# Optimization experiments

Hardware: AMD Instinct MI355X
Metric: run time of the kernel (lower is better)

The kernel has to match this reference:

```python
import jax, jax.numpy as jnp
import numpy as np

HEADS = 8
KD = 64  # key_dim
VD = 64  # value_dim


def _conv1x1(W, b, x):
    # 1x1 conv == per-pixel matmul over channels. W: [out, in], x: [b, in, h, w]
    return jnp.einsum('oc,bchw->bohw', W, x) + b[:, None, None]


def setup_inputs() -> dict:
    key = jax.random.key(0)
    ks = jax.random.split(key, 9)
    B, C, H, W = 4, 128, 128, 128
    s = 0.02
    return {
        'x':  jax.random.normal(ks[0], (B, C, H, W), jnp.float32),
        'Wq': jax.random.normal(ks[1], (KD * HEADS, C), jnp.float32) * s,
        'bq': jax.random.normal(ks[2], (KD * HEADS,), jnp.float32) * s,
        'Wk': jax.random.normal(ks[3], (KD * HEADS, C), jnp.float32) * s,
        'bk': jax.random.normal(ks[4], (KD * HEADS,), jnp.float32) * s,
        'Wv': jax.random.normal(ks[5], (VD * HEADS, C), jnp.float32) * s,
        'bv': jax.random.normal(ks[6], (VD * HEADS,), jnp.float32) * s,
        'Wo': jax.random.normal(ks[7], (C, VD * HEADS), jnp.float32) * s,
        'bo': jax.random.normal(ks[8], (C,), jnp.float32) * s,
    }


def reference(x, Wq, bq, Wk, bk, Wv, bv, Wo, bo):
    B, C, H, W = x.shape
    n = H * W
    scale = KD ** -0.25
    # projections -> [b, heads, dim, n]
    q = _conv1x1(Wq, bq, x).reshape(B, HEADS, KD, n) * scale
    k = _conv1x1(Wk, bk, x).reshape(B, HEADS, KD, n) * scale
    v = _conv1x1(Wv, bv, x).reshape(B, HEADS, VD, n)
    # linear attention: softmax k over tokens (n), softmax q over key dim (d)
    k = jax.nn.softmax(k, axis=-1)
    q = jax.nn.softmax(q, axis=-2)
    ctx = jnp.einsum('bhdn,bhen->bhde', k, v)   # [b, h, kd, vd] small context
    out = jnp.einsum('bhdn,bhde->bhen', q, ctx)  # [b, h, vd, n]
    out = out.reshape(B, HEADS * VD, H, W)
    return _conv1x1(Wo, bo, out)
```

## Files before the change

kernel.cpp:

```cpp
#include <hip/hip_runtime.h>

typedef unsigned short u16;
typedef __bf16 bf16x8 __attribute__((ext_vector_type(8)));
typedef float f32x4 __attribute__((ext_vector_type(4)));

#define N_ 16384
#define SCALE 0.35355339059327379f

__device__ __forceinline__ u16 f2bf(float f){
  union { float f; unsigned int i; } v; v.f = f;
  unsigned int b = v.i;
  return (u16)((b + 0x7FFFu + ((b >> 16) & 1u)) >> 16);
}
__device__ __forceinline__ unsigned int pack2bf(float a, float b){
  return ((unsigned int)f2bf(b) << 16) | (unsigned int)f2bf(a);
}

__global__ __launch_bounds__(256) void prep(const float* __restrict__ Wq,
    const float* __restrict__ bq, const float* __restrict__ Wk,
    const float* __restrict__ bk, const float* __restrict__ Wv,
    const float* __restrict__ bv, u16* __restrict__ wkvf, u16* __restrict__ wqf,
    float* __restrict__ bkv, float* __restrict__ bqs){
  const int T = blockIdx.x * 256 + threadIdx.x;
  if (T < 1024){
    int jj = T & 127, h = T >> 7;
    bkv[T] = (jj < 64) ? SCALE * bk[h * 64 + jj] : bv[h * 64 + jj - 64];
  } else if (T < 1536){
    bqs[T - 1024] = SCALE * bq[T - 1024];
  }
  const float* src; float sc; u16* dst;
  if (T < 16384){
    int l = T & 63, f = T >> 6;
    int ks = f & 3, jt = (f >> 2) & 7, h = f >> 5;
    int jj = 16 * jt + (l & 15);
    int k0 = ks * 32 + (l >> 4) * 8;
    if (jj < 64){ src = Wk + (size_t)(h * 64 + jj) * 128 + k0; sc = SCALE; }
    else        { src = Wv + (size_t)(h * 64 + jj - 64) * 128 + k0; sc = 1.f; }
    dst = wkvf + (size_t)f * 512 + l * 8;
  } else {
    int T2 = T - 16384;
    int l = T2 & 63, f = T2 >> 6;
    int ks = f & 3, dt = (f >> 2) & 3, h = f >> 4;
    int d = 16 * dt + (l & 15);
    int k0 = ks * 32 + (l >> 4) * 8;
    src = Wq + (size_t)(h * 64 + d) * 128 + k0; sc = SCALE;
    dst = wqf + (size_t)f * 512 + l * 8;
  }
  float4 a = *(const float4*)src, c = *(const float4*)(src + 4);
  ushort4 o0, o1;
  o0.x = f2bf(sc * a.x); o0.y = f2bf(sc * a.y); o0.z = f2bf(sc * a.z); o0.w = f2bf(sc * a.w);
  o1.x = f2bf(sc * c.x); o1.y = f2bf(sc * c.y); o1.z = f2bf(sc * c.z); o1.w = f2bf(sc * c.w);
  *(ushort4*)dst = o0; *(ushort4*)(dst + 4) = o1;
}

__global__ __launch_bounds__(256) void convx(const float* __restrict__ x,
                                             u16* __restrict__ xt){
  const int tid = threadIdx.x;
  const int b = blockIdx.y;
  const int kq = tid >> 6;
  const int t0 = blockIdx.x * 128 + 2 * (tid & 63);
  const float* xp = x + (size_t)(b * 128 + kq * 32) * N_ + t0;
  u16* dst = xt + (size_t)(b * N_ + t0) * 128;
#pragma unroll
  for (int gi = 0; gi < 4; gi++){
    float2 v[8];
#pragma unroll
    for (int j = 0; j < 8; j++)
      v[j] = *(const float2*)(xp + (size_t)(gi * 8 + j) * N_);
    const int g = kq * 4 + gi;
    {
      uint4 o;
      o.x = pack2bf(v[0].x, v[1].x); o.y = pack2bf(v[2].x, v[3].x);
      o.z = pack2bf(v[4].x, v[5].x); o.w = pack2bf(v[6].x, v[7].x);
      *(uint4*)(dst + ((g ^ (t0 & 15)) * 8)) = o;
    }
    {
      uint4 o;
      o.x = pack2bf(v[0].y, v[1].y); o.y = pack2bf(v[2].y, v[3].y);
      o.z = pack2bf(v[4].y, v[5].y); o.w = pack2bf(v[6].y, v[7].y);
      const int t = t0 + 1;
      *(uint4*)(dst + 128 + ((g ^ (t & 15)) * 8)) = o;
    }
  }
}

__global__ __launch_bounds__(256, 2) void kvctx(const u16* __restrict__ xt,
    const u16* __restrict__ wkvf, const float* __restrict__ bkv,
    float* __restrict__ pctx, float* __restrict__ prs){
  __shared__ u16 smem[32768];
  const int tid = threadIdx.x;
  const int chunk = blockIdx.x, h = blockIdx.y, b = blockIdx.z;
  const int w = tid >> 6, l = tid & 63, r15 = l & 15, q = l >> 4;
  const int th = w & 1, jh = w >> 1;

  bf16x8 wf[4][4];
#pragma unroll
  for (int ni = 0; ni < 4; ni++)
#pragma unroll
    for (int ks = 0; ks < 4; ks++)
      wf[ni][ks] = *(const bf16x8*)(wkvf +
          (size_t)((h * 8 + 4 * jh + ni) * 4 + ks) * 512 + l * 8);
  float barr[4];
#pragma unroll
  for (int ni = 0; ni < 4; ni++)
    barr[ni] = bkv[h * 128 + jh * 64 + 16 * ni + r15];

  const size_t tok0 = (size_t)b * N_ + chunk * 512;
  const char* gbase = (const char*)(xt + tok0 * 128);
  u16* sekv = smem + 16384;

#define STAGE(sub_)                                                            \
  {                                                                            \
    const char* gs = gbase + (size_t)(sub_)*32768 + w * 8192 + l * 16;         \
    char* ls = (char*)smem + w * 8192;                                         \
    _Pragma("unroll")                                                          \
    for (int p = 0; p < 8; p++)                                                \
      __builtin_amdgcn_global_load_lds(                                        \
          (const __attribute__((address_space(1))) void*)(gs + p * 1024),      \
          (__attribute__((address_space(3))) void*)(ls + p * 1024), 16, 0, 0); \
  }

  STAGE(0);
  __syncthreads();

  f32x4 acc2[4][4] = {};
  float rs[4] = {0.f, 0.f, 0.f, 0.f};

  for (int sub = 0; sub < 4; sub++){
    f32x4 acc1[4][4] = {};
#pragma unroll
    for (int ks = 0; ks < 4; ks++){
      bf16x8 xa[4];
#pragma unroll
      for (int mi = 0; mi < 4; mi++){
        int t = th * 64 + 16 * mi + r15;
        xa[mi] = *(const bf16x8*)&smem[t * 128 + (((ks * 4 + q) ^ r15) * 8)];
      }
#pragma unroll
      for (int mi = 0; mi < 4; mi++)
#pragma unroll
        for (int ni = 0; ni < 4; ni++)
          acc1[mi][ni] = __builtin_amdgcn_mfma_f32_16x16x32_bf16(
              xa[mi], wf[ni][ks], acc1[mi][ni], 0, 0, 0);
    }
#pragma unroll
    for (int ni = 0; ni < 4; ni++){
      const float bb = barr[ni];
      const int j = jh * 64 + 16 * ni + r15;
      float ps = 0.f;
#pragma unroll
      for (int mi = 0; mi < 4; mi++){
        float vals[4];
#pragma unroll
        for (int r = 0; r < 4; r++) vals[r] = acc1[mi][ni][r] + bb;
        if (jh == 0){
#pragma unroll
          for (int r = 0; r < 4; r++){ vals[r] = __expf(vals[r]); ps += vals[r]; }
        }
        uint2 pk;
        pk.x = pack2bf(vals[0], vals[1]);
        pk.y = pack2bf(vals[2], vals[3]);
        int g8 = 16 * th + 4 * mi + q;
        int g8s = g8 ^ (2 * r15);
        *(uint2*)&sekv[j * 128 + g8s * 4] = pk;
      }
      if (jh == 0){
        ps += __shfl_xor(ps, 16); ps += __shfl_xor(ps, 32);
        rs[ni] += ps;
      }
    }
    __syncthreads();
    if (sub < 3) STAGE(sub + 1);
    {
      bf16x8 ka[4], va[4];
      const int g8s = (8 * w + 2 * q) ^ (2 * r15);
#pragma unroll
      for (int mi2 = 0; mi2 < 4; mi2++){
        int d = 16 * mi2 + r15;
        ka[mi2] = *(const bf16x8*)&sekv[d * 128 + g8s * 4];
      }
#pragma unroll
      for (int ni2 = 0; ni2 < 4; ni2++){
        int e = 16 * ni2 + r15;
        va[ni2] = *(const bf16x8*)&sekv[(64 + e) * 128 + g8s * 4];
      }
#pragma unroll
      for (int mi2 = 0; mi2 < 4; mi2++)
#pragma unroll
        for (int ni2 = 0; ni2 < 4; ni2++)
          acc2[mi2][ni2] = __builtin_amdgcn_mfma_f32_16x16x32_bf16(
              ka[mi2], va[ni2], acc2[mi2][ni2], 0, 0, 0);
    }
    __syncthreads();
  }
#undef STAGE
  float* fb = (float*)smem;
#pragma unroll
  for (int mi2 = 0; mi2 < 4; mi2++)
#pragma unroll
    for (int ni2 = 0; ni2 < 4; ni2++)
#pragma unroll
      for (int r = 0; r < 4; r++){
        int d = 16 * mi2 + 4 * q + r, e = 16 * ni2 + r15;
        fb[w * 4096 + d * 64 + e] = acc2[mi2][ni2][r];
      }
  __syncthreads();
  {
    float* dst = pctx + ((size_t)((b * 8 + h) * 32 + chunk)) * 4096 + tid * 16;
#pragma unroll
    for (int i = 0; i < 4; i++){
      int o = tid * 16 + 4 * i;
      float4 a = *(const float4*)(fb + o);
      float4 c = *(const float4*)(fb + 4096 + o);
      float4 d = *(const float4*)(fb + 8192 + o);
      float4 e = *(const float4*)(fb + 12288 + o);
      float4 s;
      s.x = a.x + c.x + d.x + e.x; s.y = a.y + c.y + d.y + e.y;
      s.z = a.z + c.z + d.z + e.z; s.w = a.w + c.w + d.w + e.w;
      *(float4*)(dst + 4 * i) = s;
    }
  }
  if (jh == 0 && q == 0){
    float* rb = prs + ((size_t)((b * 8 + h) * 32 + chunk)) * 128 + th * 64;
#pragma unroll
    for (int ni = 0; ni < 4; ni++) rb[16 * ni + r15] = rs[ni];
  }
}

__global__ __launch_bounds__(256) void ctxred(const float* __restrict__ pctx,
    const float* __restrict__ prs, float* __restrict__ ctx,
    float* __restrict__ rowsum){
  const int bh = blockIdx.x, s = blockIdx.y, tid = threadIdx.x;
  const float2* base = (const float2*)(pctx + (size_t)bh * 32 * 4096 + s * 512) + tid;
  float2 acc = {0.f, 0.f};
#pragma unroll 4
  for (int t = 0; t < 32; t++){
    float2 v = base[t * 2048];
    acc.x += v.x; acc.y += v.y;
  }
  *((float2*)(ctx + (size_t)bh * 4096 + s * 512) + tid) = acc;
  if (s == 0 && tid < 64){
    const float* rb = prs + (size_t)bh * 32 * 128 + tid;
    float sm = 0.f;
    for (int t = 0; t < 32; t++) sm += rb[t * 128] + rb[t * 128 + 64];
    rowsum[bh * 64 + tid] = sm;
  }
}

__global__ __launch_bounds__(256) void mker(const float* __restrict__ ctx,
    const float* __restrict__ Wo, const float* __restrict__ rowsum,
    u16* __restrict__ mtf){
  __shared__ float ctxh[64][68];
  __shared__ float woht[64][132];
  const int tid = threadIdx.x;
  const int h = blockIdx.x, b = blockIdx.y;
  const int bh = b * 8 + h;
  const int e4 = tid & 15, r0 = tid >> 4;
#pragma unroll
  for (int p = 0; p < 4; p++){
    int d = r0 + p * 16;
    float4 v = *(const float4*)(ctx + ((size_t)bh * 64 + d) * 64 + 4 * e4);
    *(float4*)&ctxh[d][4 * e4] = v;
  }
#pragma unroll
  for (int p = 0; p < 8; p++){
    int c = r0 + p * 16;
    float4 v = *(const float4*)(Wo + (size_t)c * 512 + h * 64 + 4 * e4);
    woht[4 * e4 + 0][c] = v.x; woht[4 * e4 + 1][c] = v.y;
    woht[4 * e4 + 2][c] = v.z; woht[4 * e4 + 3][c] = v.w;
  }
  __syncthreads();
  const int cg = tid & 3, d = tid >> 2;
  const float inv = 1.f / rowsum[bh * 64 + d];
  float acc[32];
#pragma unroll
  for (int cc = 0; cc < 32; cc++) acc[cc] = 0.f;
  for (int e = 0; e < 64; e++){
    float cv = ctxh[d][e];
#pragma unroll
    for (int cc = 0; cc < 32; cc++) acc[cc] += cv * woht[e][cg + 4 * cc];
  }
  const int ks = d >> 5, lq = ((d >> 3) & 3) << 4, el = d & 7;
#pragma unroll
  for (int cc = 0; cc < 32; cc++){
    int c = cg + 4 * cc;
    mtf[((size_t)(bh * 8 + (c >> 4)) * 2 + ks) * 512 + ((c & 15) | lq) * 8 + el]
        = f2bf(inv * acc[cc]);
  }
}

__global__ __launch_bounds__(256, 3) void qout(const u16* __restrict__ xt,
    const u16* __restrict__ wqf, const float* __restrict__ bqs,
    const u16* __restrict__ mtf, const float* __restrict__ bo,
    float* __restrict__ out){
  __shared__ u16 smP[4][16 * 64];
  const int tid = threadIdx.x;
  const int tt = blockIdx.x, b = blockIdx.y;
  const int w = tid >> 6, l = tid & 63, r15 = l & 15, q = l >> 4;
  const int t0 = tt * 64;
  const int m7 = 2 * (r15 & 7);
  const int t = t0 + w * 16 + r15;

  bf16x8 xb[4];
#pragma unroll
  for (int ks = 0; ks < 4; ks++)
    xb[ks] = *(const bf16x8*)(xt + (size_t)(b * N_ + t) * 128 +
                              (((ks * 4 + q) ^ r15) * 8));

  u16* sp = smP[w];
  f32x4 acc3[8] = {};
  for (int h = 0; h < 8; h++){
    float bq_[4][4];
#pragma unroll
    for (int mi = 0; mi < 4; mi++){
      float4 v = *(const float4*)(bqs + h * 64 + 16 * mi + 4 * q);
      bq_[mi][0] = v.x; bq_[mi][1] = v.y; bq_[mi][2] = v.z; bq_[mi][3] = v.w;
    }
    f32x4 acc1[4] = {};
#pragma unroll
    for (int ks = 0; ks < 4; ks++){
      bf16x8 wqv[4];
#pragma unroll
      for (int mi = 0; mi < 4; mi++)
        wqv[mi] = *(const bf16x8*)(wqf +
            (size_t)((h * 4 + mi) * 4 + ks) * 512 + l * 8);
#pragma unroll
      for (int mi = 0; mi < 4; mi++)
        acc1[mi] = __builtin_amdgcn_mfma_f32_16x16x32_bf16(
            wqv[mi], xb[ks], acc1[mi], 0, 0, 0);
    }
    {
      float ps = 0.f;
#pragma unroll
      for (int mi = 0; mi < 4; mi++)
#pragma unroll
        for (int r = 0; r < 4; r++){
          float e = __expf(acc1[mi][r] + bq_[mi][r]);
          acc1[mi][r] = e; ps += e;
        }
      ps += __shfl_xor(ps, 16); ps += __shfl_xor(ps, 32);
      const float ci = 1.f / ps;
#pragma unroll
      for (int mi = 0; mi < 4; mi++){
        uint2 pk;
        pk.x = pack2bf(acc1[mi][0] * ci, acc1[mi][1] * ci);
        pk.y = pack2bf(acc1[mi][2] * ci, acc1[mi][3] * ci);
        int g8s = (4 * mi + q) ^ m7;
        *(uint2*)&sp[r15 * 64 + g8s * 4] = pk;
      }
    }
#pragma unroll
    for (int ks2 = 0; ks2 < 2; ks2++){
      const int g8s = (8 * ks2 + 2 * q) ^ m7;
      bf16x8 pb = *(const bf16x8*)&sp[r15 * 64 + g8s * 4];
#pragma unroll
      for (int half = 0; half < 2; half++){
        bf16x8 mf[4];
#pragma unroll
        for (int mm = 0; mm < 4; mm++)
          mf[mm] = *(const bf16x8*)(mtf +
              ((size_t)((b * 8 + h) * 8 + half * 4 + mm) * 2 + ks2) * 512 + l * 8);
#pragma unroll
        for (int mm = 0; mm < 4; mm++)
          acc3[half * 4 + mm] = __builtin_amdgcn_mfma_f32_16x16x32_bf16(
              mf[mm], pb, acc3[half * 4 + mm], 0, 0, 0);
      }
    }
  }
#pragma unroll
  for (int mi = 0; mi < 8; mi++){
    float4 bv = *(const float4*)(bo + 16 * mi + 4 * q);
    float bs[4] = {bv.x, bv.y, bv.z, bv.w};
#pragma unroll
    for (int r = 0; r < 4; r++){
      int c = 16 * mi + 4 * q + r;
      out[(size_t)(b * 128 + c) * N_ + t] = acc3[mi][r] + bs[r];
    }
  }
}

extern "C" void kernel_launch(void* const* d_in, const int* in_sizes, int n_in,
                              void* d_out, int out_size, void* d_ws, size_t ws_size,
                              hipStream_t stream){
  const float* x  = (const float*)d_in[0];
  const float* Wq = (const float*)d_in[1];
  const float* bq = (const float*)d_in[2];
  const float* Wk = (const float*)d_in[3];
  const float* bk = (const float*)d_in[4];
  const float* Wv = (const float*)d_in[5];
  const float* bv = (const float*)d_in[6];
  const float* Wo = (const float*)d_in[7];
  const float* bo = (const float*)d_in[8];
  float* out = (float*)d_out;

  char* ws = (char*)d_ws;
  u16*   xt     = (u16*)ws;
  u16*   wkvf   = (u16*)(ws + 16777216);
  u16*   wqf    = (u16*)(ws + 17039360);
  u16*   mtf    = (u16*)(ws + 17170432);
  float* bkv    = (float*)(ws + 17694720);
  float* bqs    = (float*)(ws + 17698816);
  float* rowsum = (float*)(ws + 17700864);
  float* ctx    = (float*)(ws + 17709056);
  float* pctx   = (float*)(ws + 18233344);
  float* prs    = (float*)(ws + 35010560);

  prep <<<96, 256, 0, stream>>>(Wq, bq, Wk, bk, Wv, bv, wkvf, wqf, bkv, bqs);
  convx<<<dim3(128, 4), 256, 0, stream>>>(x, xt);
  kvctx<<<dim3(32, 8, 4), 256, 0, stream>>>(xt, wkvf, bkv, pctx, prs);
  ctxred<<<dim3(32, 8), 256, 0, stream>>>(pctx, prs, ctx, rowsum);
  mker <<<dim3(8, 4), 256, 0, stream>>>(ctx, Wo, rowsum, mtf);
  qout <<<dim3(256, 4), 256, 0, stream>>>(xt, wqf, bqs, mtf, bo, out);
}
```

Baseline: 202.8 us.

## Merge prep/convx and ctxred/mker kernels, software-pipeline qout heads, use hw bf16 cvt

Folds the weight-prep and x-transpose kernels into one launch, and folds the partial-context reduction into the M-matrix kernel, removing two launches and the ctx/rowsum round trips through global memory. Replaces the manual bf16 rounding with the v_cvt_pk_bf16_f32 instruction. In kvctx, the next-stage load is moved earlier between split barriers. qout is double-buffered across head pairs so the Q projection of the next head overlaps the softmax and output MFMA of the current one, and its occupancy hint is raised to 4. The redmker reduction now runs on only 32 blocks, which may serialize the pctx reads, and the extra live accumulators in qout add register pressure.

```diff
diff --git a/kernel.cpp b/kernel.cpp
--- a/kernel.cpp
+++ b/kernel.cpp
@@ -12,16 +12,50 @@
   unsigned int b = v.i;
   return (u16)((b + 0x7FFFu + ((b >> 16) & 1u)) >> 16);
 }
-__device__ __forceinline__ unsigned int pack2bf(float a, float b){
-  return ((unsigned int)f2bf(b) << 16) | (unsigned int)f2bf(a);
-}
-
-__global__ __launch_bounds__(256) void prep(const float* __restrict__ Wq,
+__device__ __forceinline__ unsigned int cvtpk(float a, float b){
+  unsigned int r;
+  asm("v_cvt_pk_bf16_f32 %0, %1, %2" : "=v"(r) : "v"(a), "v"(b));
+  return r;
+}
+
+__global__ __launch_bounds__(256) void pconvx(const float* __restrict__ x,
+    u16* __restrict__ xt, const float* __restrict__ Wq,
     const float* __restrict__ bq, const float* __restrict__ Wk,
     const float* __restrict__ bk, const float* __restrict__ Wv,
     const float* __restrict__ bv, u16* __restrict__ wkvf, u16* __restrict__ wqf,
     float* __restrict__ bkv, float* __restrict__ bqs){
-  const int T = blockIdx.x * 256 + threadIdx.x;
+  const int tid = threadIdx.x;
+  const int bid = blockIdx.x;
+  if (bid < 512){
+    const int b = bid >> 7;
+    const int kq = tid >> 6;
+    const int t0 = (bid & 127) * 128 + 2 * (tid & 63);
+    const float* xp = x + (size_t)(b * 128 + kq * 32) * N_ + t0;
+    u16* dst = xt + (size_t)(b * N_ + t0) * 128;
+#pragma unroll
+    for (int gi = 0; gi < 4; gi++){
+      float2 v[8];
+#pragma unroll
+      for (int j = 0; j < 8; j++)
+        v[j] = *(const float2*)(xp + (size_t)(gi * 8 + j) * N_);
+      const int g = kq * 4 + gi;
+      {
+        uint4 o;
+        o.x = cvtpk(v[0].x, v[1].x); o.y = cvtpk(v[2].x, v[3].x);
+        o.z = cvtpk(v[4].x, v[5].x); o.w = cvtpk(v[6].x, v[7].x);
+        *(uint4*)(dst + ((g ^ (t0 & 15)) * 8)) = o;
+      }
+      {
+        uint4 o;
+        o.x = cvtpk(v[0].y, v[1].y); o.y = cvtpk(v[2].y, v[3].y);
+        o.z = cvtpk(v[4].y, v[5].y); o.w = cvtpk(v[6].y, v[7].y);
+        const int t = t0 + 1;
+        *(uint4*)(dst + 128 + ((g ^ (t & 15)) * 8)) = o;
+      }
+    }
+    return;
+  }
+  const int T = (bid - 512) * 256 + tid;
   if (T < 1024){
     int jj = T & 127, h = T >> 7;
     bkv[T] = (jj < 64) ? SCALE * bk[h * 64 + jj] : bv[h * 64 + jj - 64];
@@ -53,37 +87,6 @@
   *(ushort4*)dst = o0; *(ushort4*)(dst + 4) = o1;
 }
 
-__global__ __launch_bounds__(256) void convx(const float* __restrict__ x,
-                                             u16* __restrict__ xt){
-  const int tid = threadIdx.x;
-  const int b = blockIdx.y;
-  const int kq = tid >> 6;
-  const int t0 = blockIdx.x * 128 + 2 * (tid & 63);
-  const float* xp = x + (size_t)(b * 128 + kq * 32) * N_ + t0;
-  u16* dst = xt + (size_t)(b * N_ + t0) * 128;
-#pragma unroll
-  for (int gi = 0; gi < 4; gi++){
-    float2 v[8];
-#pragma unroll
-    for (int j = 0; j < 8; j++)
-      v[j] = *(const float2*)(xp + (size_t)(gi * 8 + j) * N_);
-    const int g = kq * 4 + gi;
-    {
-      uint4 o;
-      o.x = pack2bf(v[0].x, v[1].x); o.y = pack2bf(v[2].x, v[3].x);
-      o.z = pack2bf(v[4].x, v[5].x); o.w = pack2bf(v[6].x, v[7].x);
-      *(uint4*)(dst + ((g ^ (t0 & 15)) * 8)) = o;
-    }
-    {
-      uint4 o;
-      o.x = pack2bf(v[0].y, v[1].y); o.y = pack2bf(v[2].y, v[3].y);
-      o.z = pack2bf(v[4].y, v[5].y); o.w = pack2bf(v[6].y, v[7].y);
-      const int t = t0 + 1;
-      *(uint4*)(dst + 128 + ((g ^ (t & 15)) * 8)) = o;
-    }
-  }
-}
-
 __global__ __launch_bounds__(256, 2) void kvctx(const u16* __restrict__ xt,
     const u16* __restrict__ wkvf, const float* __restrict__ bkv,
     float* __restrict__ pctx, float* __restrict__ prs){
@@ -143,6 +146,9 @@
           acc1[mi][ni] = __builtin_amdgcn_mfma_f32_16x16x32_bf16(
               xa[mi], wf[ni][ks], acc1[mi][ni], 0, 0, 0);
     }
+    asm volatile("s_waitcnt lgkmcnt(0)" ::: "memory");
+    __builtin_amdgcn_s_barrier();
+    if (sub < 3) STAGE(sub + 1);
 #pragma unroll
     for (int ni = 0; ni < 4; ni++){
       const float bb = barr[ni];
@@ -158,8 +164,8 @@
           for (int r = 0; r < 4; r++){ vals[r] = __expf(vals[r]); ps += vals[r]; }
         }
         uint2 pk;
-        pk.x = pack2bf(vals[0], vals[1]);
-        pk.y = pack2bf(vals[2], vals[3]);
+        pk.x = cvtpk(vals[0], vals[1]);
+        pk.y = cvtpk(vals[2], vals[3]);
         int g8 = 16 * th + 4 * mi + q;
         int g8s = g8 ^ (2 * r15);
         *(uint2*)&sekv[j * 128 + g8s * 4] = pk;
@@ -169,8 +175,8 @@
         rs[ni] += ps;
       }
     }
-    __syncthreads();
-    if (sub < 3) STAGE(sub + 1);
+    asm volatile("s_waitcnt lgkmcnt(0)" ::: "memory");
+    __builtin_amdgcn_s_barrier();
     {
       bf16x8 ka[4], va[4];
       const int g8s = (8 * w + 2 * q) ^ (2 * r15);
@@ -227,51 +233,53 @@
   }
 }
 
-__global__ __launch_bounds__(256) void ctxred(const float* __restrict__ pctx,
-    const float* __restrict__ prs, float* __restrict__ ctx,
-    float* __restrict__ rowsum){
-  const int bh = blockIdx.x, s = blockIdx.y, tid = threadIdx.x;
-  const float2* base = (const float2*)(pctx + (size_t)bh * 32 * 4096 + s * 512) + tid;
-  float2 acc = {0.f, 0.f};
-#pragma unroll 4
-  for (int t = 0; t < 32; t++){
-    float2 v = base[t * 2048];
-    acc.x += v.x; acc.y += v.y;
-  }
-  *((float2*)(ctx + (size_t)bh * 4096 + s * 512) + tid) = acc;
-  if (s == 0 && tid < 64){
-    const float* rb = prs + (size_t)bh * 32 * 128 + tid;
-    float sm = 0.f;
-    for (int t = 0; t < 32; t++) sm += rb[t * 128] + rb[t * 128 + 64];
-    rowsum[bh * 64 + tid] = sm;
-  }
-}
-
-__global__ __launch_bounds__(256) void mker(const float* __restrict__ ctx,
-    const float* __restrict__ Wo, const float* __restrict__ rowsum,
+__global__ __launch_bounds__(256) void redmker(const float* __restrict__ pctx,
+    const float* __restrict__ prs, const float* __restrict__ Wo,
     u16* __restrict__ mtf){
   __shared__ float ctxh[64][68];
   __shared__ float woht[64][132];
+  __shared__ float rsh[64];
   const int tid = threadIdx.x;
-  const int h = blockIdx.x, b = blockIdx.y;
-  const int bh = b * 8 + h;
-  const int e4 = tid & 15, r0 = tid >> 4;
-#pragma unroll
-  for (int p = 0; p < 4; p++){
-    int d = r0 + p * 16;
-    float4 v = *(const float4*)(ctx + ((size_t)bh * 64 + d) * 64 + 4 * e4);
-    *(float4*)&ctxh[d][4 * e4] = v;
-  }
-#pragma unroll
-  for (int p = 0; p < 8; p++){
-    int c = r0 + p * 16;
-    float4 v = *(const float4*)(Wo + (size_t)c * 512 + h * 64 + 4 * e4);
-    woht[4 * e4 + 0][c] = v.x; woht[4 * e4 + 1][c] = v.y;
-    woht[4 * e4 + 2][c] = v.z; woht[4 * e4 + 3][c] = v.w;
+  const int bh = blockIdx.x;
+  const int h = bh & 7;
+  {
+    const int e4 = tid & 15, r0 = tid >> 4;
+#pragma unroll
+    for (int p = 0; p < 8; p++){
+      int c = r0 + p * 16;
+      float4 v = *(const float4*)(Wo + (size_t)c * 512 + h * 64 + 4 * e4);
+      woht[4 * e4 + 0][c] = v.x; woht[4 * e4 + 1][c] = v.y;
+      woht[4 * e4 + 2][c] = v.z; woht[4 * e4 + 3][c] = v.w;
+    }
+  }
+  {
+    const float4* base = (const float4*)(pctx + (size_t)bh * 131072) + tid * 4;
+    float4 a0 = {0,0,0,0}, a1 = {0,0,0,0}, a2 = {0,0,0,0}, a3 = {0,0,0,0};
+#pragma unroll 4
+    for (int c = 0; c < 32; c++){
+      float4 v0 = base[c * 1024 + 0], v1 = base[c * 1024 + 1];
+      float4 v2 = base[c * 1024 + 2], v3 = base[c * 1024 + 3];
+      a0.x += v0.x; a0.y += v0.y; a0.z += v0.z; a0.w += v0.w;
+      a1.x += v1.x; a1.y += v1.y; a1.z += v1.z; a1.w += v1.w;
+      a2.x += v2.x; a2.y += v2.y; a2.z += v2.z; a2.w += v2.w;
+      a3.x += v3.x; a3.y += v3.y; a3.z += v3.z; a3.w += v3.w;
+    }
+    const int d = tid >> 2, e0 = (tid & 3) * 16;
+    *(float4*)&ctxh[d][e0 + 0]  = a0;
+    *(float4*)&ctxh[d][e0 + 4]  = a1;
+    *(float4*)&ctxh[d][e0 + 8]  = a2;
+    *(float4*)&ctxh[d][e0 + 12] = a3;
+  }
+  if (tid < 64){
+    const float* rb = prs + (size_t)bh * 4096 + tid;
+    float sm = 0.f;
+#pragma unroll 4
+    for (int c = 0; c < 32; c++) sm += rb[c * 128] + rb[c * 128 + 64];
+    rsh[tid] = sm;
   }
   __syncthreads();
   const int cg = tid & 3, d = tid >> 2;
-  const float inv = 1.f / rowsum[bh * 64 + d];
+  const float inv = 1.f / rsh[d];
   float acc[32];
 #pragma unroll
   for (int cc = 0; cc < 32; cc++) acc[cc] = 0.f;
@@ -289,11 +297,11 @@
   }
 }
 
-__global__ __launch_bounds__(256, 3) void qout(const u16* __restrict__ xt,
+__global__ __launch_bounds__(256, 4) void qout(const u16* __restrict__ xt,
     const u16* __restrict__ wqf, const float* __restrict__ bqs,
     const u16* __restrict__ mtf, const float* __restrict__ bo,
     float* __restrict__ out){
-  __shared__ u16 smP[4][16 * 64];
+  __shared__ u16 smP[4][2][16 * 64];
   const int tid = threadIdx.x;
   const int tt = blockIdx.x, b = blockIdx.y;
   const int w = tid >> 6, l = tid & 63, r15 = l & 15, q = l >> 4;
@@ -307,66 +315,83 @@
     xb[ks] = *(const bf16x8*)(xt + (size_t)(b * N_ + t) * 128 +
                               (((ks * 4 + q) ^ r15) * 8));
 
-  u16* sp = smP[w];
+  u16* sp0 = smP[w][0];
+  u16* sp1 = smP[w][1];
   f32x4 acc3[8] = {};
-  for (int h = 0; h < 8; h++){
-    float bq_[4][4];
-#pragma unroll
-    for (int mi = 0; mi < 4; mi++){
-      float4 v = *(const float4*)(bqs + h * 64 + 16 * mi + 4 * q);
-      bq_[mi][0] = v.x; bq_[mi][1] = v.y; bq_[mi][2] = v.z; bq_[mi][3] = v.w;
-    }
-    f32x4 acc1[4] = {};
-#pragma unroll
-    for (int ks = 0; ks < 4; ks++){
-      bf16x8 wqv[4];
-#pragma unroll
-      for (int mi = 0; mi < 4; mi++)
-        wqv[mi] = *(const bf16x8*)(wqf +
-            (size_t)((h * 4 + mi) * 4 + ks) * 512 + l * 8);
-#pragma unroll
-      for (int mi = 0; mi < 4; mi++)
-        acc1[mi] = __builtin_amdgcn_mfma_f32_16x16x32_bf16(
-            wqv[mi], xb[ks], acc1[mi], 0, 0, 0);
-    }
-    {
-      float ps = 0.f;
-#pragma unroll
-      for (int mi = 0; mi < 4; mi++)
-#pragma unroll
-        for (int r = 0; r < 4; r++){
-          float e = __expf(acc1[mi][r] + bq_[mi][r]);
-          acc1[mi][r] = e; ps += e;
-        }
-      ps += __shfl_xor(ps, 16); ps += __shfl_xor(ps, 32);
-      const float ci = 1.f / ps;
-#pragma unroll
-      for (int mi = 0; mi < 4; mi++){
-        uint2 pk;
-        pk.x = pack2bf(acc1[mi][0] * ci, acc1[mi][1] * ci);
-        pk.y = pack2bf(acc1[mi][2] * ci, acc1[mi][3] * ci);
-        int g8s = (4 * mi + q) ^ m7;
-        *(uint2*)&sp[r15 * 64 + g8s * 4] = pk;
-      }
-    }
-#pragma unroll
-    for (int ks2 = 0; ks2 < 2; ks2++){
-      const int g8s = (8 * ks2 + 2 * q) ^ m7;
-      bf16x8 pb = *(const bf16x8*)&sp[r15 * 64 + g8s * 4];
-#pragma unroll
-      for (int half = 0; half < 2; half++){
-        bf16x8 mf[4];
-#pragma unroll
-        for (int mm = 0; mm < 4; mm++)
-          mf[mm] = *(const bf16x8*)(mtf +
-              ((size_t)((b * 8 + h) * 8 + half * 4 + mm) * 2 + ks2) * 512 + l * 8);
-#pragma unroll
-        for (int mm = 0; mm < 4; mm++)
-          acc3[half * 4 + mm] = __builtin_amdgcn_mfma_f32_16x16x32_bf16(
-              mf[mm], pb, acc3[half * 4 + mm], 0, 0, 0);
-      }
-    }
-  }
+
+#define MFMA1(h_, acc_)                                                      \
+  { _Pragma("unroll")                                                        \
+    for (int ks = 0; ks < 4; ks++){                                          \
+      bf16x8 wqv[4];                                                         \
+      _Pragma("unroll")                                                      \
+      for (int mi = 0; mi < 4; mi++)                                         \
+        wqv[mi] = *(const bf16x8*)(wqf +                                     \
+            (size_t)(((h_) * 4 + mi) * 4 + ks) * 512 + l * 8);               \
+      _Pragma("unroll")                                                      \
+      for (int mi = 0; mi < 4; mi++)                                         \
+        acc_[mi] = __builtin_amdgcn_mfma_f32_16x16x32_bf16(                  \
+            wqv[mi], xb[ks], acc_[mi], 0, 0, 0);                             \
+    } }
+
+#define SM(h_, acc_, sp_)                                                    \
+  { float ps = 0.f;                                                          \
+    _Pragma("unroll")                                                        \
+    for (int mi = 0; mi < 4; mi++){                                          \
+      float4 bv = *(const float4*)(bqs + (h_) * 64 + 16 * mi + 4 * q);       \
+      float e0 = __expf(acc_[mi][0] + bv.x);                                 \
+      float e1 = __expf(acc_[mi][1] + bv.y);                                 \
+      float e2 = __expf(acc_[mi][2] + bv.z);                                 \
+      float e3 = __expf(acc_[mi][3] + bv.w);                                 \
+      acc_[mi][0] = e0; acc_[mi][1] = e1;                                    \
+      acc_[mi][2] = e2; acc_[mi][3] = e3;                                    \
+      ps += (e0 + e1) + (e2 + e3);                                           \
+    }                                                                        \
+    ps += __shfl_xor(ps, 16); ps += __shfl_xor(ps, 32);                      \
+    const float ci = 1.f / ps;                                               \
+    _Pragma("unroll")                                                        \
+    for (int mi = 0; mi < 4; mi++){                                          \
+      uint2 pk;                                                              \
+      pk.x = cvtpk(acc_[mi][0] * ci, acc_[mi][1] * ci);                      \
+      pk.y = cvtpk(acc_[mi][2] * ci, acc_[mi][3] * ci);                      \
+      int g8s = (4 * mi + q) ^ m7;                                           \
+      *(uint2*)&sp_[r15 * 64 + g8s * 4] = pk;                                \
+    } }
+
+#define MFMA2(h_, sp_)                                                       \
+  { _Pragma("unroll")                                                        \
+    for (int ks2 = 0; ks2 < 2; ks2++){                                       \
+      const int g8s = (8 * ks2 + 2 * q) ^ m7;                                \
+      bf16x8 pb = *(const bf16x8*)&sp_[r15 * 64 + g8s * 4];                  \
+      _Pragma("unroll")                                                      \
+      for (int mm = 0; mm < 8; mm++){                                        \
+        bf16x8 mf = *(const bf16x8*)(mtf +                                   \
+            ((size_t)((b * 8 + (h_)) * 8 + mm) * 2 + ks2) * 512 + l * 8);    \
+        acc3[mm] = __builtin_amdgcn_mfma_f32_16x16x32_bf16(                  \
+            mf, pb, acc3[mm], 0, 0, 0);                                      \
+      }                                                                      \
+    } }
+
+  f32x4 acc1A[4] = {};
+  f32x4 acc1B[4];
+  MFMA1(0, acc1A);
+#pragma unroll
+  for (int hp = 0; hp < 4; hp++){
+    const int h0 = 2 * hp, h1 = 2 * hp + 1;
+#pragma unroll
+    for (int mi = 0; mi < 4; mi++) acc1B[mi] = (f32x4){0.f, 0.f, 0.f, 0.f};
+    SM(h0, acc1A, sp0);
+    MFMA1(h1, acc1B);
+    MFMA2(h0, sp0);
+#pragma unroll
+    for (int mi = 0; mi < 4; mi++) acc1A[mi] = (f32x4){0.f, 0.f, 0.f, 0.f};
+    SM(h1, acc1B, sp1);
+    if (hp < 3) MFMA1(h0 + 2, acc1A);
+    MFMA2(h1, sp1);
+  }
+#undef MFMA1
+#undef SM
+#undef MFMA2
+
 #pragma unroll
   for (int mi = 0; mi < 8; mi++){
     float4 bv = *(const float4*)(bo + 16 * mi + 4 * q);
@@ -400,15 +425,12 @@
   u16*   mtf    = (u16*)(ws + 17170432);
   float* bkv    = (float*)(ws + 17694720);
   float* bqs    = (float*)(ws + 17698816);
-  float* rowsum = (float*)(ws + 17700864);
-  float* ctx    = (float*)(ws + 17709056);
   float* pctx   = (float*)(ws + 18233344);
   float* prs    = (float*)(ws + 35010560);
 
-  prep <<<96, 256, 0, stream>>>(Wq, bq, Wk, bk, Wv, bv, wkvf, wqf, bkv, bqs);
-  convx<<<dim3(128, 4), 256, 0, stream>>>(x, xt);
-  kvctx<<<dim3(32, 8, 4), 256, 0, stream>>>(xt, wkvf, bkv, pctx, prs);
-  ctxred<<<dim3(32, 8), 256, 0, stream>>>(pctx, prs, ctx, rowsum);
-  mker <<<dim3(8, 4), 256, 0, stream>>>(ctx, Wo, rowsum, mtf);
-  qout <<<dim3(256, 4), 256, 0, stream>>>(xt, wqf, bqs, mtf, bo, out);
-}
+  pconvx <<<608, 256, 0, stream>>>(x, xt, Wq, bq, Wk, bk, Wv, bv,
+                                   wkvf, wqf, bkv, bqs);
+  kvctx  <<<dim3(32, 8, 4), 256, 0, stream>>>(xt, wkvf, bkv, pctx, prs);
+  redmker<<<32, 256, 0, stream>>>(pctx, prs, Wo, mtf);
+  qout   <<<dim3(256, 4), 256, 0, stream>>>(xt, wqf, bqs, mtf, bo, out);
+}
```

After: 208.3 us. 1.03x slower.

## Fuse prep/convert and reduce/mker kernels, widen kvctx and qout to 512 threads

Applied to the files above, without the earlier changes.

Merges the weight-prep and x-transpose kernels into one launch, and merges the ctx partial reduction with the mker kernel, cutting the chain from six launches to four. kvctx moves to 512 threads with each wave owning a smaller output tile, loads weights from global inside the loop instead of holding them in registers, and issues the next stage prefetch earlier. qout splits the heads across two wave groups and sums their results through shared memory. Bf16 packing now uses the hardware v_cvt_pk_bf16_f32 instruction, which may round differently from the software routine, and the partial sums in kvctx are reduced differently.

```diff
diff --git a/kernel.cpp b/kernel.cpp
--- a/kernel.cpp
+++ b/kernel.cpp
@@ -12,16 +12,50 @@
   unsigned int b = v.i;
   return (u16)((b + 0x7FFFu + ((b >> 16) & 1u)) >> 16);
 }
-__device__ __forceinline__ unsigned int pack2bf(float a, float b){
-  return ((unsigned int)f2bf(b) << 16) | (unsigned int)f2bf(a);
-}
-
-__global__ __launch_bounds__(256) void prep(const float* __restrict__ Wq,
+__device__ __forceinline__ unsigned int cvtpk(float a, float b){
+  unsigned int r;
+  asm("v_cvt_pk_bf16_f32 %0, %1, %2" : "=v"(r) : "v"(a), "v"(b));
+  return r;
+}
+
+__global__ __launch_bounds__(256) void pconvx(const float* __restrict__ x,
+    u16* __restrict__ xt, const float* __restrict__ Wq,
     const float* __restrict__ bq, const float* __restrict__ Wk,
     const float* __restrict__ bk, const float* __restrict__ Wv,
     const float* __restrict__ bv, u16* __restrict__ wkvf, u16* __restrict__ wqf,
     float* __restrict__ bkv, float* __restrict__ bqs){
-  const int T = blockIdx.x * 256 + threadIdx.x;
+  const int tid = threadIdx.x;
+  const int bid = blockIdx.x;
+  if (bid < 512){
+    const int b = bid >> 7;
+    const int kq = tid >> 6;
+    const int t0 = (bid & 127) * 128 + 2 * (tid & 63);
+    const float* xp = x + (size_t)(b * 128 + kq * 32) * N_ + t0;
+    u16* dst = xt + (size_t)(b * N_ + t0) * 128;
+#pragma unroll
+    for (int gi = 0; gi < 4; gi++){
+      float2 v[8];
+#pragma unroll
+      for (int j = 0; j < 8; j++)
+        v[j] = *(const float2*)(xp + (size_t)(gi * 8 + j) * N_);
+      const int g = kq * 4 + gi;
+      {
+        uint4 o;
+        o.x = cvtpk(v[0].x, v[1].x); o.y = cvtpk(v[2].x, v[3].x);
+        o.z = cvtpk(v[4].x, v[5].x); o.w = cvtpk(v[6].x, v[7].x);
+        *(uint4*)(dst + ((g ^ (t0 & 15)) * 8)) = o;
+      }
+      {
+        uint4 o;
+        o.x = cvtpk(v[0].y, v[1].y); o.y = cvtpk(v[2].y, v[3].y);
+        o.z = cvtpk(v[4].y, v[5].y); o.w = cvtpk(v[6].y, v[7].y);
+        const int t = t0 + 1;
+        *(uint4*)(dst + 128 + ((g ^ (t & 15)) * 8)) = o;
+      }
+    }
+    return;
+  }
+  const int T = (bid - 512) * 256 + tid;
   if (T < 1024){
     int jj = T & 127, h = T >> 7;
     bkv[T] = (jj < 64) ? SCALE * bk[h * 64 + jj] : bv[h * 64 + jj - 64];
@@ -53,53 +87,16 @@
   *(ushort4*)dst = o0; *(ushort4*)(dst + 4) = o1;
 }
 
-__global__ __launch_bounds__(256) void convx(const float* __restrict__ x,
-                                             u16* __restrict__ xt){
-  const int tid = threadIdx.x;
-  const int b = blockIdx.y;
-  const int kq = tid >> 6;
-  const int t0 = blockIdx.x * 128 + 2 * (tid & 63);
-  const float* xp = x + (size_t)(b * 128 + kq * 32) * N_ + t0;
-  u16* dst = xt + (size_t)(b * N_ + t0) * 128;
-#pragma unroll
-  for (int gi = 0; gi < 4; gi++){
-    float2 v[8];
-#pragma unroll
-    for (int j = 0; j < 8; j++)
-      v[j] = *(const float2*)(xp + (size_t)(gi * 8 + j) * N_);
-    const int g = kq * 4 + gi;
-    {
-      uint4 o;
-      o.x = pack2bf(v[0].x, v[1].x); o.y = pack2bf(v[2].x, v[3].x);
-      o.z = pack2bf(v[4].x, v[5].x); o.w = pack2bf(v[6].x, v[7].x);
-      *(uint4*)(dst + ((g ^ (t0 & 15)) * 8)) = o;
-    }
-    {
-      uint4 o;
-      o.x = pack2bf(v[0].y, v[1].y); o.y = pack2bf(v[2].y, v[3].y);
-      o.z = pack2bf(v[4].y, v[5].y); o.w = pack2bf(v[6].y, v[7].y);
-      const int t = t0 + 1;
-      *(uint4*)(dst + 128 + ((g ^ (t & 15)) * 8)) = o;
-    }
-  }
-}
-
-__global__ __launch_bounds__(256, 2) void kvctx(const u16* __restrict__ xt,
+__global__ __launch_bounds__(512, 4) void kvctx(const u16* __restrict__ xt,
     const u16* __restrict__ wkvf, const float* __restrict__ bkv,
     float* __restrict__ pctx, float* __restrict__ prs){
   __shared__ u16 smem[32768];
   const int tid = threadIdx.x;
   const int chunk = blockIdx.x, h = blockIdx.y, b = blockIdx.z;
   const int w = tid >> 6, l = tid & 63, r15 = l & 15, q = l >> 4;
-  const int th = w & 1, jh = w >> 1;
-
-  bf16x8 wf[4][4];
-#pragma unroll
-  for (int ni = 0; ni < 4; ni++)
-#pragma unroll
-    for (int ks = 0; ks < 4; ks++)
-      wf[ni][ks] = *(const bf16x8*)(wkvf +
-          (size_t)((h * 8 + 4 * jh + ni) * 4 + ks) * 512 + l * 8);
+  const int th = w & 3, jh = w >> 2;
+  const int ni2 = w & 3, m0 = 2 * (w >> 2);
+
   float barr[4];
 #pragma unroll
   for (int ni = 0; ni < 4; ni++)
@@ -111,10 +108,10 @@
 
 #define STAGE(sub_)                                                            \
   {                                                                            \
-    const char* gs = gbase + (size_t)(sub_)*32768 + w * 8192 + l * 16;         \
-    char* ls = (char*)smem + w * 8192;                                         \
+    const char* gs = gbase + (size_t)(sub_)*32768 + w * 4096 + l * 16;         \
+    char* ls = (char*)smem + w * 4096;                                         \
     _Pragma("unroll")                                                          \
-    for (int p = 0; p < 8; p++)                                                \
+    for (int p = 0; p < 4; p++)                                                \
       __builtin_amdgcn_global_load_lds(                                        \
           (const __attribute__((address_space(1))) void*)(gs + p * 1024),      \
           (__attribute__((address_space(3))) void*)(ls + p * 1024), 16, 0, 0); \
@@ -123,33 +120,41 @@
   STAGE(0);
   __syncthreads();
 
-  f32x4 acc2[4][4] = {};
+  f32x4 acc2[2] = {{0.f,0.f,0.f,0.f},{0.f,0.f,0.f,0.f}};
   float rs[4] = {0.f, 0.f, 0.f, 0.f};
 
   for (int sub = 0; sub < 4; sub++){
-    f32x4 acc1[4][4] = {};
+    f32x4 acc1[2][4] = {};
 #pragma unroll
     for (int ks = 0; ks < 4; ks++){
-      bf16x8 xa[4];
-#pragma unroll
-      for (int mi = 0; mi < 4; mi++){
-        int t = th * 64 + 16 * mi + r15;
+      bf16x8 wfv[4];
+#pragma unroll
+      for (int ni = 0; ni < 4; ni++)
+        wfv[ni] = *(const bf16x8*)(wkvf +
+            (size_t)((h * 8 + jh * 4 + ni) * 4 + ks) * 512 + l * 8);
+      bf16x8 xa[2];
+#pragma unroll
+      for (int mi = 0; mi < 2; mi++){
+        int t = th * 32 + 16 * mi + r15;
         xa[mi] = *(const bf16x8*)&smem[t * 128 + (((ks * 4 + q) ^ r15) * 8)];
       }
 #pragma unroll
-      for (int mi = 0; mi < 4; mi++)
+      for (int mi = 0; mi < 2; mi++)
 #pragma unroll
         for (int ni = 0; ni < 4; ni++)
           acc1[mi][ni] = __builtin_amdgcn_mfma_f32_16x16x32_bf16(
-              xa[mi], wf[ni][ks], acc1[mi][ni], 0, 0, 0);
-    }
+              xa[mi], wfv[ni], acc1[mi][ni], 0, 0, 0);
+    }
+    asm volatile("s_waitcnt lgkmcnt(0)" ::: "memory");
+    __builtin_amdgcn_s_barrier();
+    if (sub < 3) STAGE(sub + 1);
 #pragma unroll
     for (int ni = 0; ni < 4; ni++){
       const float bb = barr[ni];
       const int j = jh * 64 + 16 * ni + r15;
       float ps = 0.f;
 #pragma unroll
-      for (int mi = 0; mi < 4; mi++){
+      for (int mi = 0; mi < 2; mi++){
         float vals[4];
 #pragma unroll
         for (int r = 0; r < 4; r++) vals[r] = acc1[mi][ni][r] + bb;
@@ -158,9 +163,9 @@
           for (int r = 0; r < 4; r++){ vals[r] = __expf(vals[r]); ps += vals[r]; }
         }
         uint2 pk;
-        pk.x = pack2bf(vals[0], vals[1]);
-        pk.y = pack2bf(vals[2], vals[3]);
-        int g8 = 16 * th + 4 * mi + q;
+        pk.x = cvtpk(vals[0], vals[1]);
+        pk.y = cvtpk(vals[2], vals[3]);
+        int g8 = 8 * th + 4 * mi + q;
         int g8s = g8 ^ (2 * r15);
         *(uint2*)&sekv[j * 128 + g8s * 4] = pk;
       }
@@ -169,109 +174,91 @@
         rs[ni] += ps;
       }
     }
+    asm volatile("s_waitcnt lgkmcnt(0)" ::: "memory");
+    __builtin_amdgcn_s_barrier();
+#pragma unroll
+    for (int ks2 = 0; ks2 < 4; ks2++){
+      const int goff = (((8 * ks2 + 2 * q) ^ (2 * r15)) * 4);
+      bf16x8 va  = *(const bf16x8*)&sekv[(64 + 16 * ni2 + r15) * 128 + goff];
+      bf16x8 ka0 = *(const bf16x8*)&sekv[(16 * m0 + r15) * 128 + goff];
+      bf16x8 ka1 = *(const bf16x8*)&sekv[(16 * (m0 + 1) + r15) * 128 + goff];
+      acc2[0] = __builtin_amdgcn_mfma_f32_16x16x32_bf16(ka0, va, acc2[0], 0, 0, 0);
+      acc2[1] = __builtin_amdgcn_mfma_f32_16x16x32_bf16(ka1, va, acc2[1], 0, 0, 0);
+    }
     __syncthreads();
-    if (sub < 3) STAGE(sub + 1);
-    {
-      bf16x8 ka[4], va[4];
-      const int g8s = (8 * w + 2 * q) ^ (2 * r15);
-#pragma unroll
-      for (int mi2 = 0; mi2 < 4; mi2++){
-        int d = 16 * mi2 + r15;
-        ka[mi2] = *(const bf16x8*)&sekv[d * 128 + g8s * 4];
-      }
-#pragma unroll
-      for (int ni2 = 0; ni2 < 4; ni2++){
-        int e = 16 * ni2 + r15;
-        va[ni2] = *(const bf16x8*)&sekv[(64 + e) * 128 + g8s * 4];
-      }
-#pragma unroll
-      for (int mi2 = 0; mi2 < 4; mi2++)
-#pragma unroll
-        for (int ni2 = 0; ni2 < 4; ni2++)
-          acc2[mi2][ni2] = __builtin_amdgcn_mfma_f32_16x16x32_bf16(
-              ka[mi2], va[ni2], acc2[mi2][ni2], 0, 0, 0);
+  }
+#undef STAGE
+  {
+    float* dst = pctx + ((size_t)((b * 8 + h) * 32 + chunk)) * 4096;
+#pragma unroll
+    for (int p = 0; p < 2; p++)
+#pragma unroll
+      for (int r = 0; r < 4; r++){
+        int d = 16 * (m0 + p) + 4 * q + r, e = 16 * ni2 + r15;
+        dst[d * 64 + e] = acc2[p][r];
+      }
+  }
+  {
+    float* rsb = (float*)smem;
+    if (jh == 0 && q == 0){
+#pragma unroll
+      for (int ni = 0; ni < 4; ni++) rsb[th * 64 + 16 * ni + r15] = rs[ni];
     }
     __syncthreads();
-  }
-#undef STAGE
-  float* fb = (float*)smem;
-#pragma unroll
-  for (int mi2 = 0; mi2 < 4; mi2++)
-#pragma unroll
-    for (int ni2 = 0; ni2 < 4; ni2++)
-#pragma unroll
-      for (int r = 0; r < 4; r++){
-        int d = 16 * mi2 + 4 * q + r, e = 16 * ni2 + r15;
-        fb[w * 4096 + d * 64 + e] = acc2[mi2][ni2][r];
-      }
-  __syncthreads();
-  {
-    float* dst = pctx + ((size_t)((b * 8 + h) * 32 + chunk)) * 4096 + tid * 16;
-#pragma unroll
-    for (int i = 0; i < 4; i++){
-      int o = tid * 16 + 4 * i;
-      float4 a = *(const float4*)(fb + o);
-      float4 c = *(const float4*)(fb + 4096 + o);
-      float4 d = *(const float4*)(fb + 8192 + o);
-      float4 e = *(const float4*)(fb + 12288 + o);
-      float4 s;
-      s.x = a.x + c.x + d.x + e.x; s.y = a.y + c.y + d.y + e.y;
-      s.z = a.z + c.z + d.z + e.z; s.w = a.w + c.w + d.w + e.w;
-      *(float4*)(dst + 4 * i) = s;
-    }
-  }
-  if (jh == 0 && q == 0){
-    float* rb = prs + ((size_t)((b * 8 + h) * 32 + chunk)) * 128 + th * 64;
-#pragma unroll
-    for (int ni = 0; ni < 4; ni++) rb[16 * ni + r15] = rs[ni];
-  }
-}
-
-__global__ __launch_bounds__(256) void ctxred(const float* __restrict__ pctx,
-    const float* __restrict__ prs, float* __restrict__ ctx,
-    float* __restrict__ rowsum){
-  const int bh = blockIdx.x, s = blockIdx.y, tid = threadIdx.x;
-  const float2* base = (const float2*)(pctx + (size_t)bh * 32 * 4096 + s * 512) + tid;
-  float2 acc = {0.f, 0.f};
-#pragma unroll 4
-  for (int t = 0; t < 32; t++){
-    float2 v = base[t * 2048];
-    acc.x += v.x; acc.y += v.y;
-  }
-  *((float2*)(ctx + (size_t)bh * 4096 + s * 512) + tid) = acc;
-  if (s == 0 && tid < 64){
-    const float* rb = prs + (size_t)bh * 32 * 128 + tid;
-    float sm = 0.f;
-    for (int t = 0; t < 32; t++) sm += rb[t * 128] + rb[t * 128 + 64];
-    rowsum[bh * 64 + tid] = sm;
-  }
-}
-
-__global__ __launch_bounds__(256) void mker(const float* __restrict__ ctx,
-    const float* __restrict__ Wo, const float* __restrict__ rowsum,
+    if (tid < 64){
+      float s = rsb[tid] + rsb[64 + tid] + rsb[128 + tid] + rsb[192 + tid];
+      prs[((size_t)((b * 8 + h) * 32 + chunk)) * 64 + tid] = s;
+    }
+  }
+}
+
+__global__ __launch_bounds__(256) void redmker(const float* __restrict__ pctx,
+    const float* __restrict__ prs, const float* __restrict__ Wo,
     u16* __restrict__ mtf){
   __shared__ float ctxh[64][68];
   __shared__ float woht[64][132];
+  __shared__ float rsh[64];
   const int tid = threadIdx.x;
-  const int h = blockIdx.x, b = blockIdx.y;
-  const int bh = b * 8 + h;
-  const int e4 = tid & 15, r0 = tid >> 4;
-#pragma unroll
-  for (int p = 0; p < 4; p++){
-    int d = r0 + p * 16;
-    float4 v = *(const float4*)(ctx + ((size_t)bh * 64 + d) * 64 + 4 * e4);
-    *(float4*)&ctxh[d][4 * e4] = v;
-  }
-#pragma unroll
-  for (int p = 0; p < 8; p++){
-    int c = r0 + p * 16;
-    float4 v = *(const float4*)(Wo + (size_t)c * 512 + h * 64 + 4 * e4);
-    woht[4 * e4 + 0][c] = v.x; woht[4 * e4 + 1][c] = v.y;
-    woht[4 * e4 + 2][c] = v.z; woht[4 * e4 + 3][c] = v.w;
+  const int bh = blockIdx.x;
+  const int h = bh & 7;
+  {
+    const int e4 = tid & 15, r0 = tid >> 4;
+#pragma unroll
+    for (int p = 0; p < 8; p++){
+      int c = r0 + p * 16;
+      float4 v = *(const float4*)(Wo + (size_t)c * 512 + h * 64 + 4 * e4);
+      woht[4 * e4 + 0][c] = v.x; woht[4 * e4 + 1][c] = v.y;
+      woht[4 * e4 + 2][c] = v.z; woht[4 * e4 + 3][c] = v.w;
+    }
+  }
+  {
+    const float4* base = (const float4*)(pctx + (size_t)bh * 131072) + tid * 4;
+    float4 a0 = {0,0,0,0}, a1 = {0,0,0,0}, a2 = {0,0,0,0}, a3 = {0,0,0,0};
+#pragma unroll 4
+    for (int c = 0; c < 32; c++){
+      float4 v0 = base[c * 1024 + 0], v1 = base[c * 1024 + 1];
+      float4 v2 = base[c * 1024 + 2], v3 = base[c * 1024 + 3];
+      a0.x += v0.x; a0.y += v0.y; a0.z += v0.z; a0.w += v0.w;
+      a1.x += v1.x; a1.y += v1.y; a1.z += v1.z; a1.w += v1.w;
+      a2.x += v2.x; a2.y += v2.y; a2.z += v2.z; a2.w += v2.w;
+      a3.x += v3.x; a3.y += v3.y; a3.z += v3.z; a3.w += v3.w;
+    }
+    const int d = tid >> 2, e0 = (tid & 3) * 16;
+    *(float4*)&ctxh[d][e0 + 0]  = a0;
+    *(float4*)&ctxh[d][e0 + 4]  = a1;
+    *(float4*)&ctxh[d][e0 + 8]  = a2;
+    *(float4*)&ctxh[d][e0 + 12] = a3;
+  }
+  if (tid < 64){
+    const float* rb = prs + (size_t)bh * 2048 + tid;
+    float sm = 0.f;
+#pragma unroll 4
+    for (int c = 0; c < 32; c++) sm += rb[c * 64];
+    rsh[tid] = sm;
   }
   __syncthreads();
   const int cg = tid & 3, d = tid >> 2;
-  const float inv = 1.f / rowsum[bh * 64 + d];
+  const float inv = 1.f / rsh[d];
   float acc[32];
 #pragma unroll
   for (int cc = 0; cc < 32; cc++) acc[cc] = 0.f;
@@ -289,17 +276,18 @@
   }
 }
 
-__global__ __launch_bounds__(256, 3) void qout(const u16* __restrict__ xt,
+__global__ __launch_bounds__(512, 8) void qout(const u16* __restrict__ xt,
     const u16* __restrict__ wqf, const float* __restrict__ bqs,
     const u16* __restrict__ mtf, const float* __restrict__ bo,
     float* __restrict__ out){
-  __shared__ u16 smP[4][16 * 64];
+  __shared__ __align__(16) char smraw[33792];
   const int tid = threadIdx.x;
   const int tt = blockIdx.x, b = blockIdx.y;
   const int w = tid >> 6, l = tid & 63, r15 = l & 15, q = l >> 4;
+  const int ts = w & 3, hh = w >> 2;
   const int t0 = tt * 64;
   const int m7 = 2 * (r15 & 7);
-  const int t = t0 + w * 16 + r15;
+  const int t = t0 + ts * 16 + r15;
 
   bf16x8 xb[4];
 #pragma unroll
@@ -307,9 +295,11 @@
     xb[ks] = *(const bf16x8*)(xt + (size_t)(b * N_ + t) * 128 +
                               (((ks * 4 + q) ^ r15) * 8));
 
-  u16* sp = smP[w];
+  u16* sp = (u16*)smraw + w * 1024;
   f32x4 acc3[8] = {};
-  for (int h = 0; h < 8; h++){
+#pragma unroll
+  for (int hi = 0; hi < 4; hi++){
+    const int h = hh * 4 + hi;
     float bq_[4][4];
 #pragma unroll
     for (int mi = 0; mi < 4; mi++){
@@ -343,8 +333,8 @@
 #pragma unroll
       for (int mi = 0; mi < 4; mi++){
         uint2 pk;
-        pk.x = pack2bf(acc1[mi][0] * ci, acc1[mi][1] * ci);
-        pk.y = pack2bf(acc1[mi][2] * ci, acc1[mi][3] * ci);
+        pk.x = cvtpk(acc1[mi][0] * ci, acc1[mi][1] * ci);
+        pk.y = cvtpk(acc1[mi][2] * ci, acc1[mi][3] * ci);
         int g8s = (4 * mi + q) ^ m7;
         *(uint2*)&sp[r15 * 64 + g8s * 4] = pk;
       }
@@ -367,14 +357,29 @@
       }
     }
   }
-#pragma unroll
-  for (int mi = 0; mi < 8; mi++){
-    float4 bv = *(const float4*)(bo + 16 * mi + 4 * q);
-    float bs[4] = {bv.x, bv.y, bv.z, bv.w};
-#pragma unroll
-    for (int r = 0; r < 4; r++){
-      int c = 16 * mi + 4 * q + r;
-      out[(size_t)(b * 128 + c) * N_ + t] = acc3[mi][r] + bs[r];
+  float* red = (float*)smraw;
+  __syncthreads();
+  if (hh == 1){
+#pragma unroll
+    for (int mi = 0; mi < 8; mi++){
+      float4 v;
+      v.x = acc3[mi][0]; v.y = acc3[mi][1]; v.z = acc3[mi][2]; v.w = acc3[mi][3];
+      *(float4*)&red[(ts * 16 + r15) * 132 + 16 * mi + 4 * q] = v;
+    }
+  }
+  __syncthreads();
+  if (hh == 0){
+#pragma unroll
+    for (int mi = 0; mi < 8; mi++){
+      float4 vr = *(const float4*)&red[(ts * 16 + r15) * 132 + 16 * mi + 4 * q];
+      float4 bv = *(const float4*)(bo + 16 * mi + 4 * q);
+      float rr[4] = {vr.x, vr.y, vr.z, vr.w};
+      float bs[4] = {bv.x, bv.y, bv.z, bv.w};
+#pragma unroll
+      for (int r = 0; r < 4; r++){
+        int c = 16 * mi + 4 * q + r;
+        out[(size_t)(b * 128 + c) * N_ + t] = acc3[mi][r] + rr[r] + bs[r];
+      }
     }
   }
 }
@@ -400,15 +405,12 @@
   u16*   mtf    = (u16*)(ws + 17170432);
   float* bkv    = (float*)(ws + 17694720);
   float* bqs    = (float*)(ws + 17698816);
-  float* rowsum = (float*)(ws + 17700864);
-  float* ctx    = (float*)(ws + 17709056);
   float* pctx   = (float*)(ws + 18233344);
   float* prs    = (float*)(ws + 35010560);
 
-  prep <<<96, 256, 0, stream>>>(Wq, bq, Wk, bk, Wv, bv, wkvf, wqf, bkv, bqs);
-  convx<<<dim3(128, 4), 256, 0, stream>>>(x, xt);
-  kvctx<<<dim3(32, 8, 4), 256, 0, stream>>>(xt, wkvf, bkv, pctx, prs);
-  ctxred<<<dim3(32, 8), 256, 0, stream>>>(pctx, prs, ctx, rowsum);
-  mker <<<dim3(8, 4), 256, 0, stream>>>(ctx, Wo, rowsum, mtf);
-  qout <<<dim3(256, 4), 256, 0, stream>>>(xt, wqf, bqs, mtf, bo, out);
-}
+  pconvx <<<608, 256, 0, stream>>>(x, xt, Wq, bq, Wk, bk, Wv, bv,
+                                   wkvf, wqf, bkv, bqs);
+  kvctx  <<<dim3(32, 8, 4), 512, 0, stream>>>(xt, wkvf, bkv, pctx, prs);
+  redmker<<<32, 256, 0, stream>>>(pctx, prs, Wo, mtf);
+  qout   <<<dim3(256, 4), 512, 0, stream>>>(xt, wqf, bqs, mtf, bo, out);
+}
```

After: 335.1 us. 65.2% more time.
